# Optimization experiments

Hardware: AMD Instinct MI355X
Metric: run time of the kernel (lower is better)

The kernel has to match this reference:

```python
import math
import jax, jax.numpy as jnp
import numpy as np

N_WIRES = 12
N_LAYERS = 3
BATCH = 2048
DIM = 2 ** N_WIRES


def _apply_1q(psi, U, wire):
    # psi: (B, 2^n) complex; U: (2,2) or (B,2,2)
    B = psi.shape[0]
    left = 2 ** wire
    psi = psi.reshape(B, left, 2, -1)
    if U.ndim == 3:
        psi = jnp.einsum('bij,bajc->baic', U, psi)
    else:
        psi = jnp.einsum('ij,bajc->baic', U, psi)
    return psi.reshape(B, -1)


def _apply_cnot(psi, wire):
    # CNOT on (control=wire, target=wire+1), adjacent wires
    B = psi.shape[0]
    left = 2 ** wire
    psi = psi.reshape(B, left, 2, 2, -1)
    flipped = psi[:, :, 1, ::-1, :][:, :, None]   # control=1 branch, target flipped
    psi = jnp.concatenate([psi[:, :, 0:1], flipped], axis=2)
    return psi.reshape(B, -1)


def _ry(theta):
    # RY(t) = [[cos t/2, -sin t/2],[sin t/2, cos t/2]]; theta: () or (B,)
    c = jnp.cos(theta / 2)
    s = jnp.sin(theta / 2)
    U = jnp.stack([jnp.stack([c, -s], -1), jnp.stack([s, c], -1)], -2)
    return U.astype(jnp.complex64)


def _rz(theta):
    # RZ(t) = diag(e^{-it/2}, e^{it/2}); theta scalar
    em = jnp.exp(-0.5j * theta.astype(jnp.complex64))
    ep = jnp.exp(0.5j * theta.astype(jnp.complex64))
    e00 = jnp.array([[1, 0], [0, 0]], dtype=jnp.complex64)
    e11 = jnp.array([[0, 0], [0, 1]], dtype=jnp.complex64)
    return e00 * em + e11 * ep


def _measure_z(psi):
    # <Z_w> for every wire; psi: (B, 2^n)
    B = psi.shape[0]
    p = jnp.abs(psi) ** 2
    outs = []
    for w in range(N_WIRES):
        pr = p.reshape(B, 2 ** w, 2, -1)
        outs.append(pr[:, :, 0].sum((1, 2)) - pr[:, :, 1].sum((1, 2)))
    return jnp.stack(outs, axis=-1)  # (B, n_wires)


def _forward(x, W1, b1, ry_theta, rz_theta, W2, b2):
    feat = x @ W1.T + b1                      # (B, n_wires)
    angles = jnp.tanh(feat) * math.pi         # encoding angles
    B = x.shape[0]
    psi = jnp.zeros((B, DIM), dtype=jnp.complex64).at[:, 0].set(1.0)
    # data encoding: per-sample RY on each wire
    for w in range(N_WIRES):
        psi = _apply_1q(psi, _ry(angles[:, w]), w)
    # variational layers with SHARED ry/rz params (module reuse in torch code)
    Ury = _ry(ry_theta)
    Urz = _rz(rz_theta)
    for _ in range(N_LAYERS):
        for w in range(N_WIRES):
            psi = _apply_1q(psi, Ury, w)
            psi = _apply_1q(psi, Urz, w)
        for w in range(N_WIRES - 1):
            psi = _apply_cnot(psi, w)
    z = _measure_z(psi)                        # (B, n_wires) real
    return z @ W2.T + b2                       # (B, 10) logits


def setup_inputs() -> dict:
    key = jax.random.key(0)
    ks = jax.random.split(key, 7)
    return {
        'x': jax.random.normal(ks[0], (BATCH, 784), dtype=jnp.float32),
        'W1': jax.random.normal(ks[1], (N_WIRES, 784), dtype=jnp.float32) * 0.03,
        'b1': jnp.zeros((N_WIRES,), dtype=jnp.float32),
        'ry_theta': jax.random.uniform(ks[2], (), dtype=jnp.float32) * 2 * math.pi,
        'rz_theta': jax.random.uniform(ks[3], (), dtype=jnp.float32) * 2 * math.pi,
        'W2': jax.random.normal(ks[4], (10, N_WIRES), dtype=jnp.float32) * 0.2,
        'b2': jnp.zeros((10,), dtype=jnp.float32),
    }


def reference(x, W1, b1, ry_theta, rz_theta, W2, b2):
    return _forward(x, W1, b1, ry_theta, rz_theta, W2, b2)
```

## Files before the change

### kernel.cpp

```cpp
#include <hip/hip_runtime.h>
#include <math.h>

#define NW   12
#define DIM  4096
#define TPB  256

typedef float v2f __attribute__((ext_vector_type(2)));

template<int CTRL>
__device__ __forceinline__ float fdpp(float v) {
    union { float f; int i; } u, w;
    u.f = v;
    w.i = __builtin_amdgcn_update_dpp(0, u.i, CTRL, 0xF, 0xF, false);
    return w.f;
}

__device__ __forceinline__ v2f cmulq(v2f a, v2f b) {
    return (v2f){ fmaf(a.x, b.x, -a.y * b.y), fmaf(a.x, b.y, a.y * b.x) };
}

template<int B>
__device__ __forceinline__ void ry_reg(v2f* r, float c, v2f vps, v2f vms) {
#pragma unroll
    for (int p = 0; p < 8; ++p) {
        const int i0 = ((p >> B) << (B + 1)) | (p & ((1 << B) - 1));
        const int i1 = i0 | (1 << B);
        const v2f a = r[i0], b = r[i1];
        r[i0] = __builtin_elementwise_fma(vms, b, a * c);
        r[i1] = __builtin_elementwise_fma(vps, a, b * c);
    }
}

template<int CTRL>
__device__ __forceinline__ void ry_dpp(v2f* r, float c, v2f vsp) {
#pragma unroll
    for (int k = 0; k < 16; ++k) {
        const v2f p = { fdpp<CTRL>(r[k].x), fdpp<CTRL>(r[k].y) };
        r[k] = __builtin_elementwise_fma(vsp, p, r[k] * c);
    }
}

__device__ __forceinline__ void ry_xor4(v2f* r, float c, v2f vsp) {
#pragma unroll
    for (int k = 0; k < 16; ++k) {
        const v2f p = { fdpp<0x141>(fdpp<0x1B>(r[k].x)),
                        fdpp<0x141>(fdpp<0x1B>(r[k].y)) };
        r[k] = __builtin_elementwise_fma(vsp, p, r[k] * c);
    }
}

__global__ __launch_bounds__(TPB, 4)
void qmnist_kernel(const float* __restrict__ x,  const float* __restrict__ W1,
                   const float* __restrict__ b1, const float* __restrict__ ryp,
                   const float* __restrict__ rzp, const float* __restrict__ W2,
                   const float* __restrict__ b2, float* __restrict__ out) {
    __shared__ v2f psi[DIM];
    float* smf  = (float*)psi;
    float* wred = smf;
    float* encc = smf + 48;
    float* encs = smf + 60;
    float* zfin = smf + 72;

    const int tid  = threadIdx.x;
    const int blk  = blockIdx.x;
    const int lane = tid & 63;
    const int wave = tid >> 6;

    float acc[NW];
#pragma unroll
    for (int w = 0; w < NW; ++w) acc[w] = 0.f;
    if (tid < 196) {
        const float4 xv = ((const float4*)(x + (size_t)blk * 784))[tid];
#pragma unroll
        for (int w = 0; w < NW; ++w) {
            const float4 wv = ((const float4*)(W1 + w * 784))[tid];
            acc[w] = fmaf(xv.x, wv.x, fmaf(xv.y, wv.y, fmaf(xv.z, wv.z, xv.w * wv.w)));
        }
    }
#pragma unroll
    for (int w = 0; w < NW; ++w) {
        float v = acc[w];
        v += __shfl_down(v, 32);
        v += __shfl_down(v, 16);
        v += __shfl_down(v, 8);
        v += __shfl_down(v, 4);
        v += __shfl_down(v, 2);
        v += __shfl_down(v, 1);
        if (lane == 0) wred[wave * NW + w] = v;
    }
    __syncthreads();
    if (tid < NW) {
        float feat = wred[tid] + wred[NW + tid] + wred[2 * NW + tid] + wred[3 * NW + tid] + b1[tid];
        float a = tanhf(feat) * 3.14159265358979323846f;
        float h = 0.5f * a;
        encc[tid] = cosf(h);
        encs[tid] = sinf(h);
    }
    __syncthreads();

    float hi = 1.f;
#pragma unroll
    for (int b = 0; b < 8; ++b)
        hi *= ((tid >> b) & 1) ? encs[11 - b] : encc[11 - b];
    v2f r[16];
#pragma unroll
    for (int k = 0; k < 16; ++k) {
        float f = hi;
        f *= (k & 1) ? encs[3] : encc[3];
        f *= (k & 2) ? encs[2] : encc[2];
        f *= (k & 4) ? encs[1] : encc[1];
        f *= (k & 8) ? encs[0] : encc[0];
        r[k] = (v2f){ f, 0.f };
    }

    const float ry = ryp[0], rz = rzp[0];
    const float c = cosf(0.5f * ry), s = sinf(0.5f * ry);
    const v2f vps = {  s,  s };
    const v2f vms = { -s, -s };
    const int pcT = __popc(tid);
    v2f qv[5], qp[5];
    {
        float sb, cb; __sincosf(rz * (float)(pcT - 6), &sb, &cb);
        float sd, cd; __sincosf(rz, &sd, &cd);
        qv[0] = (v2f){ cb, sb };
        const v2f step = (v2f){ cd, sd };
#pragma unroll
        for (int j = 1; j < 5; ++j) qv[j] = cmulq(qv[j - 1], step);
#pragma unroll
        for (int j = 0; j < 5; ++j) qp[j] = (v2f){ -qv[j].y, qv[j].x };
    }

    const v2f vs0 = (lane & 1) ? vps : vms;
    const v2f vs1 = (lane & 2) ? vps : vms;
    const v2f vs2 = (lane & 4) ? vps : vms;
    const v2f vs3 = (lane & 8) ? vps : vms;

    const int base_r = (tid & 15) | ((tid & 240) << 4);
    const int gt     = tid ^ (tid >> 1);

    for (int layer = 0; layer < 2; ++layer) {
        __syncthreads();

        ry_reg<0>(r, c, vps, vms); ry_reg<1>(r, c, vps, vms);
        ry_reg<2>(r, c, vps, vms); ry_reg<3>(r, c, vps, vms);

#pragma unroll
        for (int k = 0; k < 16; ++k)
            psi[(k << 8) | tid] = r[k];
        __syncthreads();
#pragma unroll
        for (int k = 0; k < 16; ++k)
            r[k] = psi[base_r | (k << 4)];

        ry_dpp<0xB1>(r, c, vs0);
        ry_dpp<0x4E>(r, c, vs1);
        ry_xor4(r, c, vs2);
        ry_dpp<0x128>(r, c, vs3);

        ry_reg<0>(r, c, vps, vms); ry_reg<1>(r, c, vps, vms);
        ry_reg<2>(r, c, vps, vms); ry_reg<3>(r, c, vps, vms);

#pragma unroll
        for (int k = 0; k < 16; ++k) {
            const int j = __popc(k);
            r[k] = __builtin_elementwise_fma((v2f){ r[k].y, r[k].y }, qp[j], qv[j] * r[k].x);
        }

#pragma unroll
        for (int k = 0; k < 16; ++k)
            psi[base_r | (k << 4)] = r[k];
        __syncthreads();
#pragma unroll
        for (int k = 0; k < 16; ++k) {
            const int gk = (k ^ (k >> 1)) & 15;
            r[k] = psi[(gt ^ ((k & 1) << 7)) | (gk << 8)];
        }
    }

    __syncthreads();
    ry_reg<0>(r, c, vps, vms); ry_reg<1>(r, c, vps, vms);
    ry_reg<2>(r, c, vps, vms); ry_reg<3>(r, c, vps, vms);
#pragma unroll
    for (int k = 0; k < 16; ++k)
        psi[(k << 8) | tid] = r[k];
    __syncthreads();
#pragma unroll
    for (int k = 0; k < 16; ++k)
        r[k] = psi[base_r | (k << 4)];
    ry_dpp<0xB1>(r, c, vs0);
    ry_dpp<0x4E>(r, c, vs1);
    ry_xor4(r, c, vs2);
    ry_dpp<0x128>(r, c, vs3);
    ry_reg<0>(r, c, vps, vms); ry_reg<1>(r, c, vps, vms);
    ry_reg<2>(r, c, vps, vms); ry_reg<3>(r, c, vps, vms);
    __syncthreads();

    float T = 0.f, Sp = 0.f, S1 = 0.f, S2 = 0.f, S3 = 0.f;
#pragma unroll
    for (int k = 0; k < 16; ++k) {
        const float pp = fmaf(r[k].x, r[k].x, r[k].y * r[k].y);
        T += pp;
        Sp += (__popc(k) & 1)        ? -pp : pp;
        S1 += (__popc(k >> 1) & 1)   ? -pp : pp;
        S2 += (__popc(k >> 2) & 1)   ? -pp : pp;
        S3 += ((k >> 3) & 1)         ? -pp : pp;
    }
    const int t1 = (tid >> 1) & 1, t2 = (tid >> 2) & 1, t3 = (tid >> 3) & 1;
    const int t4 = (tid >> 4) & 1, t5 = (tid >> 5) & 1, t6 = (tid >> 6) & 1,
              t7 = (tid >> 7) & 1;
    const int p47 = t4 ^ t5 ^ t6 ^ t7;
    float contrib[NW];
    contrib[0]  = t7                   ? -T : T;
    contrib[1]  = (t6 ^ t7)            ? -T : T;
    contrib[2]  = (t5 ^ t6 ^ t7)       ? -T : T;
    contrib[3]  = p47                  ? -T : T;
    contrib[4]  = p47                  ? -S3 : S3;
    contrib[5]  = p47                  ? -S2 : S2;
    contrib[6]  = p47                  ? -S1 : S1;
    contrib[7]  = p47                  ? -Sp : Sp;
    contrib[8]  = (t3 ^ p47)           ? -Sp : Sp;
    contrib[9]  = (t2 ^ t3 ^ p47)      ? -Sp : Sp;
    contrib[10] = (t1 ^ t2 ^ t3 ^ p47) ? -Sp : Sp;
    contrib[11] = (pcT & 1)            ? -Sp : Sp;
#pragma unroll
    for (int w = 0; w < NW; ++w) {
        float v = contrib[w];
        v += __shfl_down(v, 32);
        v += __shfl_down(v, 16);
        v += __shfl_down(v, 8);
        v += __shfl_down(v, 4);
        v += __shfl_down(v, 2);
        v += __shfl_down(v, 1);
        if (lane == 0) wred[wave * NW + w] = v;
    }
    __syncthreads();
    if (tid < NW)
        zfin[tid] = wred[tid] + wred[NW + tid] + wred[2 * NW + tid] + wred[3 * NW + tid];
    __syncthreads();

    if (tid < 10) {
        float o = b2[tid];
#pragma unroll
        for (int w = 0; w < NW; ++w)
            o = fmaf(zfin[w], W2[tid * NW + w], o);
        out[(size_t)blk * 10 + tid] = o;
    }
}

extern "C" void kernel_launch(void* const* d_in, const int* in_sizes, int n_in,
                              void* d_out, int out_size, void* d_ws, size_t ws_size,
                              hipStream_t stream) {
    const float* x   = (const float*)d_in[0];
    const float* W1  = (const float*)d_in[1];
    const float* b1  = (const float*)d_in[2];
    const float* ry  = (const float*)d_in[3];
    const float* rz  = (const float*)d_in[4];
    const float* W2  = (const float*)d_in[5];
    const float* b2  = (const float*)d_in[6];
    float* out = (float*)d_out;

    const int batch = in_sizes[0] / 784;
    qmnist_kernel<<<batch, TPB, 0, stream>>>(x, W1, b1, ry, rz, W2, b2, out);
}
```

Baseline: 113.8 us.

## Unroll layers with per-layer Gray-code shared-memory layouts to cut syncs

Unrolls the three variational layers and gives each stage its own permuted shared-memory addressing (Gray-code bases GA1, GA2, bs2). The CNOT-chain permutation is folded into these address maps instead of being realised by a separate reload. This is meant to remove the extra sync and store/load round trip that sat between the loop and the final layer. The hand-derived index maps are error-prone, and the address patterns may change LDS bank conflicts.

```diff
diff --git a/kernel.cpp b/kernel.cpp
--- a/kernel.cpp
+++ b/kernel.cpp
@@ -135,64 +135,65 @@
     const v2f vs2 = (lane & 4) ? vps : vms;
     const v2f vs3 = (lane & 8) ? vps : vms;
 
-    const int base_r = (tid & 15) | ((tid & 240) << 4);
-    const int gt     = tid ^ (tid >> 1);
-
-    for (int layer = 0; layer < 2; ++layer) {
-        __syncthreads();
-
-        ry_reg<0>(r, c, vps, vms); ry_reg<1>(r, c, vps, vms);
-        ry_reg<2>(r, c, vps, vms); ry_reg<3>(r, c, vps, vms);
-
-#pragma unroll
-        for (int k = 0; k < 16; ++k)
-            psi[(k << 8) | tid] = r[k];
-        __syncthreads();
-#pragma unroll
-        for (int k = 0; k < 16; ++k)
-            r[k] = psi[base_r | (k << 4)];
-
-        ry_dpp<0xB1>(r, c, vs0);
-        ry_dpp<0x4E>(r, c, vs1);
-        ry_xor4(r, c, vs2);
-        ry_dpp<0x128>(r, c, vs3);
-
-        ry_reg<0>(r, c, vps, vms); ry_reg<1>(r, c, vps, vms);
-        ry_reg<2>(r, c, vps, vms); ry_reg<3>(r, c, vps, vms);
-
-#pragma unroll
-        for (int k = 0; k < 16; ++k) {
-            const int j = __popc(k);
-            r[k] = __builtin_elementwise_fma((v2f){ r[k].y, r[k].y }, qp[j], qv[j] * r[k].x);
-        }
-
-#pragma unroll
-        for (int k = 0; k < 16; ++k)
-            psi[base_r | (k << 4)] = r[k];
-        __syncthreads();
-#pragma unroll
-        for (int k = 0; k < 16; ++k) {
-            const int gk = (k ^ (k >> 1)) & 15;
-            r[k] = psi[(gt ^ ((k & 1) << 7)) | (gk << 8)];
-        }
-    }
-
-    __syncthreads();
-    ry_reg<0>(r, c, vps, vms); ry_reg<1>(r, c, vps, vms);
-    ry_reg<2>(r, c, vps, vms); ry_reg<3>(r, c, vps, vms);
-#pragma unroll
-    for (int k = 0; k < 16; ++k)
-        psi[(k << 8) | tid] = r[k];
-    __syncthreads();
-#pragma unroll
-    for (int k = 0; k < 16; ++k)
-        r[k] = psi[base_r | (k << 4)];
-    ry_dpp<0xB1>(r, c, vs0);
-    ry_dpp<0x4E>(r, c, vs1);
-    ry_xor4(r, c, vs2);
-    ry_dpp<0x128>(r, c, vs3);
-    ry_reg<0>(r, c, vps, vms); ry_reg<1>(r, c, vps, vms);
-    ry_reg<2>(r, c, vps, vms); ry_reg<3>(r, c, vps, vms);
+    const int A    = (tid & 15) | ((tid & 240) << 4);
+    const int gt   = tid ^ (tid >> 1);
+    const int GA1  = A ^ (A >> 1);
+    const int GA2  = A ^ (A >> 2);
+    const int bs2  = tid ^ (tid >> 2);
+
+#define GREG() { ry_reg<0>(r, c, vps, vms); ry_reg<1>(r, c, vps, vms); \
+                 ry_reg<2>(r, c, vps, vms); ry_reg<3>(r, c, vps, vms); }
+#define GDPP() { ry_dpp<0xB1>(r, c, vs0); ry_dpp<0x4E>(r, c, vs1); \
+                 ry_xor4(r, c, vs2);      ry_dpp<0x128>(r, c, vs3); }
+#define RZF()  _Pragma("unroll") for (int k = 0; k < 16; ++k) { \
+                 const int j = __popc(k); \
+                 r[k] = __builtin_elementwise_fma((v2f){ r[k].y, r[k].y }, qp[j], qv[j] * r[k].x); }
+#define S0_Y(k)   (((k) << 8) | tid)
+#define S0_A(k)   (A | ((k) << 4))
+#define S1_Y(k)   ((gt ^ (((k) & 1) << 7)) | ((((k) ^ ((k) >> 1)) & 15) << 8))
+#define S1_A(k)   (GA1 ^ (((k) << 4) ^ ((k) << 3)))
+#define S2_Y(k)   (bs2 ^ (((k) & 3) << 6) ^ ((((k) ^ ((k) >> 2)) & 15) << 8))
+#define S2_A(k)   (GA2 ^ (((k) << 4) ^ ((k) << 2)))
+
+    __syncthreads();
+    GREG();
+#pragma unroll
+    for (int k = 0; k < 16; ++k) psi[S0_Y(k)] = r[k];
+    __syncthreads();
+#pragma unroll
+    for (int k = 0; k < 16; ++k) r[k] = psi[S0_A(k)];
+    GDPP();
+    GREG();
+    RZF();
+#pragma unroll
+    for (int k = 0; k < 16; ++k) psi[S0_A(k)] = r[k];
+    __syncthreads();
+#pragma unroll
+    for (int k = 0; k < 16; ++k) r[k] = psi[S1_Y(k)];
+
+    GREG();
+#pragma unroll
+    for (int k = 0; k < 16; ++k) psi[S1_Y(k)] = r[k];
+    __syncthreads();
+#pragma unroll
+    for (int k = 0; k < 16; ++k) r[k] = psi[S1_A(k)];
+    GDPP();
+    GREG();
+    RZF();
+#pragma unroll
+    for (int k = 0; k < 16; ++k) psi[S1_A(k)] = r[k];
+    __syncthreads();
+#pragma unroll
+    for (int k = 0; k < 16; ++k) r[k] = psi[S2_Y(k)];
+
+    GREG();
+#pragma unroll
+    for (int k = 0; k < 16; ++k) psi[S2_Y(k)] = r[k];
+    __syncthreads();
+#pragma unroll
+    for (int k = 0; k < 16; ++k) r[k] = psi[S2_A(k)];
+    GDPP();
+    GREG();
     __syncthreads();
 
     float T = 0.f, Sp = 0.f, S1 = 0.f, S2 = 0.f, S3 = 0.f;
```

Result: no change. 113.3 us (-0.4%).
